# Optimization experiments

Measured on AMD Instinct MI355X. Metric: run time of the kernel, lower is better.

Reference implementation:

```python
import jax, jax.numpy as jnp
import numpy as np

B, S, DK, H = 4, 4096, 768, 64

def setup_inputs() -> dict:
    key = jax.random.key(0)
    ks = jax.random.split(key, 5)
    scale = 1.0 / np.sqrt(DK)
    x = jax.random.normal(ks[0], (B, S, DK), dtype=jnp.float32)
    Wq = jax.random.normal(ks[1], (H, DK), dtype=jnp.float32) * scale
    bq = jnp.zeros((H,), dtype=jnp.float32)
    Wv = jax.random.normal(ks[2], (H, DK), dtype=jnp.float32) * scale
    bv = jnp.zeros((H,), dtype=jnp.float32)
    return {"x": x, "Wq": Wq, "bq": bq, "Wv": Wv, "bv": bv}

def reference(x, Wq, bq, Wv, bv):
    # Faithful to source: k uses the QUERY projection (source bug), scale = d_k**-0.5 with d_k = input dim
    dk = x.shape[-1]
    q = jnp.einsum('bsd,hd->bsh', x, Wq) + bq  # [B,S,H]
    k = jnp.einsum('bsd,hd->bsh', x, Wq) + bq  # same projection as q
    v = jnp.einsum('bsd,hd->bsh', x, Wv) + bv
    score = jnp.einsum('bqh,bkh->bqk', q, k) * (dk ** -0.5)  # [B,S,S]
    prob = jax.nn.softmax(score, axis=-1)
    out = jnp.einsum('bqk,bkh->bqh', prob, v)  # [B,S,H]
    return out
```

## Files before the change

### kernel.cpp

```cpp
#include <hip/hip_runtime.h>
#include <hip/hip_bf16.h>
#include <stdint.h>
#include <math.h>


typedef unsigned short u16;
typedef __attribute__((ext_vector_type(8))) short bf16x8;
typedef __attribute__((ext_vector_type(4))) float f32x4;

#define MFMA16(a,b,c) __builtin_amdgcn_mfma_f32_16x16x32_bf16((a),(b),(c),0,0,0)

__device__ __forceinline__ u16 f2bf(float f) {
  union { float f; uint32_t u; } v; v.f = f;
  uint32_t u = v.u;
  return (u16)((u + 0x7FFFu + ((u >> 16) & 1u)) >> 16);
}

__device__ __forceinline__ bf16x8 ldsfrag(const u16* lds, int row, int k) {
  return *(const bf16x8*)(lds + row * 64 + (k ^ ((row & 7) << 3)));
}

__device__ __forceinline__ void gload_lds16(const void* g, void* l) {
  __builtin_amdgcn_global_load_lds(
      (__attribute__((address_space(1))) void*)g,
      (__attribute__((address_space(3))) void*)l, 16, 0, 0);
}

struct Regs { float4 r[12]; };

__device__ __forceinline__ void issue_loads(Regs& R, const float* xp,
                                            const float* qp, const float* vp,
                                            int ks) {
  const float4* a = (const float4*)(xp + (ks << 6));
  const float4* b = (const float4*)(qp + (ks << 6));
  const float4* c = (const float4*)(vp + (ks << 6));
  R.r[0] = a[0]; R.r[1] = a[1]; R.r[2] = a[2]; R.r[3] = a[3];
  R.r[4] = b[0]; R.r[5] = b[1]; R.r[6] = b[2]; R.r[7] = b[3];
  R.r[8] = c[0]; R.r[9] = c[1]; R.r[10] = c[2]; R.r[11] = c[3];
}

__device__ __forceinline__ void cvt8(const float4& a, const float4& b, bf16x8& o) {
  o[0] = (short)f2bf(a.x); o[1] = (short)f2bf(a.y);
  o[2] = (short)f2bf(a.z); o[3] = (short)f2bf(a.w);
  o[4] = (short)f2bf(b.x); o[5] = (short)f2bf(b.y);
  o[6] = (short)f2bf(b.z); o[7] = (short)f2bf(b.w);
}

__device__ __forceinline__ void cvt_store(const Regs& R, u16* xrow, u16* qrow,
                                          u16* vrow, int scol, int xsw) {
  bf16x8 lo, hi;
  cvt8(R.r[0], R.r[1], lo);  cvt8(R.r[2], R.r[3], hi);
  *(bf16x8*)(xrow + (scol ^ xsw)) = lo;
  *(bf16x8*)(xrow + ((scol + 8) ^ xsw)) = hi;
  cvt8(R.r[4], R.r[5], lo);  cvt8(R.r[6], R.r[7], hi);
  *(bf16x8*)(qrow + (scol ^ xsw)) = lo;
  *(bf16x8*)(qrow + ((scol + 8) ^ xsw)) = hi;
  cvt8(R.r[8], R.r[9], lo);  cvt8(R.r[10], R.r[11], hi);
  *(bf16x8*)(vrow + (scol ^ xsw)) = lo;
  *(bf16x8*)(vrow + ((scol + 8) ^ xsw)) = hi;
}

__global__ __launch_bounds__(256) void proj_k(
    const float* __restrict__ x, const float* __restrict__ Wq,
    const float* __restrict__ bq, const float* __restrict__ Wv,
    const float* __restrict__ bv, u16* __restrict__ qbf,
    u16* __restrict__ vtbf, float qscale)
{
  __shared__ __align__(16) u16 xs[2][4096];
  __shared__ __align__(16) u16 wqs[2][4096];
  __shared__ __align__(16) u16 wvs[2][4096];
  const int tid = threadIdx.x;
  const int lane = tid & 63;
  const int w = tid >> 6;
  const int l15 = lane & 15, lg = lane >> 4;
  const int s0 = blockIdx.x * 64;

  f32x4 acc[2][4];
#pragma unroll
  for (int i = 0; i < 2; i++)
#pragma unroll
    for (int n = 0; n < 4; n++) acc[i][n] = (f32x4){0.f, 0.f, 0.f, 0.f};

  const int srow = tid >> 2;
  const int scol = (tid & 3) << 4;
  const int xsw = (srow & 7) << 3;
  const float* xsrc = x + (size_t)(s0 + srow) * 768 + scol;
  const float* qsrc = Wq + (size_t)srow * 768 + scol;
  const float* vsrc = Wv + (size_t)srow * 768 + scol;

  Regs A, B;
  issue_loads(A, xsrc, qsrc, vsrc, 0);
  issue_loads(B, xsrc, qsrc, vsrc, 1);
  asm volatile("s_waitcnt vmcnt(12)" ::: "memory");
  cvt_store(A, &xs[0][srow * 64], &wqs[0][srow * 64], &wvs[0][srow * 64], scol, xsw);

#pragma unroll
  for (int ks = 0; ks < 12; ++ks) {
    const int b = ks & 1;
    if (ks + 2 < 12) {
      if (b) issue_loads(B, xsrc, qsrc, vsrc, ks + 2);
      else   issue_loads(A, xsrc, qsrc, vsrc, ks + 2);
    }
    asm volatile("s_waitcnt lgkmcnt(0)" ::: "memory");
    __builtin_amdgcn_s_barrier();
    __builtin_amdgcn_sched_barrier(0);

    const u16* xt = xs[b];
    const u16* qt = wqs[b];
    const u16* vt = wvs[b];
#pragma unroll
    for (int kk = 0; kk < 2; ++kk) {
      const int k = kk * 32 + lg * 8;
      if (w < 2) {
        bf16x8 a0 = ldsfrag(xt, (2 * w + 0) * 16 + l15, k);
        bf16x8 a1 = ldsfrag(xt, (2 * w + 1) * 16 + l15, k);
#pragma unroll
        for (int n = 0; n < 4; n++) {
          bf16x8 bb = ldsfrag(qt, n * 16 + l15, k);
          acc[0][n] = MFMA16(a0, bb, acc[0][n]);
          acc[1][n] = MFMA16(a1, bb, acc[1][n]);
        }
      } else {
        bf16x8 a0 = ldsfrag(vt, (2 * (w - 2) + 0) * 16 + l15, k);
        bf16x8 a1 = ldsfrag(vt, (2 * (w - 2) + 1) * 16 + l15, k);
#pragma unroll
        for (int n = 0; n < 4; n++) {
          bf16x8 bb = ldsfrag(xt, n * 16 + l15, k);
          acc[0][n] = MFMA16(a0, bb, acc[0][n]);
          acc[1][n] = MFMA16(a1, bb, acc[1][n]);
        }
      }
    }
    if (ks + 1 < 12) {
      if (ks < 10) asm volatile("s_waitcnt vmcnt(12)" ::: "memory");
      else         asm volatile("s_waitcnt vmcnt(0)" ::: "memory");
      u16* xd = &xs[b ^ 1][srow * 64];
      u16* qd = &wqs[b ^ 1][srow * 64];
      u16* vd = &wvs[b ^ 1][srow * 64];
      if (b) cvt_store(A, xd, qd, vd, scol, xsw);
      else   cvt_store(B, xd, qd, vd, scol, xsw);
    }
  }

  if (w < 2) {
#pragma unroll
    for (int i = 0; i < 2; i++)
#pragma unroll
      for (int n = 0; n < 4; n++) {
        const int h = n * 16 + l15;
        const float bias = bq[h];
#pragma unroll
        for (int r = 0; r < 4; r++) {
          const int sg = s0 + (2 * w + i) * 16 + lg * 4 + r;
          qbf[(size_t)sg * 64 + h] = f2bf((acc[i][n][r] + bias) * qscale);
        }
      }
  } else {
    const int b = s0 >> 12;
    const int sloc = s0 & 4095;
#pragma unroll
    for (int i = 0; i < 2; i++)
#pragma unroll
      for (int n = 0; n < 4; n++) {
        const int scg = sloc + n * 16 + l15;
#pragma unroll
        for (int r = 0; r < 4; r++) {
          const int h = (2 * (w - 2) + i) * 16 + lg * 4 + r;
          vtbf[(size_t)(b * 64 + h) * 4096 + scg] = f2bf(acc[i][n][r] + bv[h]);
        }
      }
  }
}

__global__ __launch_bounds__(512) void attn_k(
    const u16* __restrict__ qbf, const u16* __restrict__ vtbf,
    float* __restrict__ out)
{
  __shared__ __align__(16) u16 smem[3 * 8192 + 8 * 640];
  u16* pl = smem + 3 * 8192;
  const int tid = threadIdx.x;
  const int lane = tid & 63;
  const int w = tid >> 6;
  const int wq = w & 3, wk = w >> 2;
  const int l15 = lane & 15, lg = lane >> 4;
  const int b = blockIdx.y;
  const int q0 = blockIdx.x << 6;

  bf16x8 qf[2];
  {
    const u16* qr = qbf + (size_t)(b * 4096 + q0 + wq * 16 + l15) * 64 + lg * 8;
    qf[0] = *(const bf16x8*)(qr);
    qf[1] = *(const bf16x8*)(qr + 32);
  }

  f32x4 oacc[4];
#pragma unroll
  for (int i = 0; i < 4; i++) oacc[i] = (f32x4){0.f, 0.f, 0.f, 0.f};
  float lacc[4] = {0.f, 0.f, 0.f, 0.f};

  const int o = tid << 4;
  const int krow = o >> 7;
  const int ksw = o ^ ((krow & 7) << 4);
  const char* kbase = (const char*)qbf + (size_t)(b * 4096) * 128;
  const char* vbase = (const char*)vtbf + (size_t)(b * 64 + krow) * 8192 + (ksw & 127);

  const int NT = 64;
  auto stage = [&](int t, int s3) {
    char* kd = (char*)smem + s3 * 16384 + o;
    gload_lds16(kbase + (size_t)t * 8192 + ksw, kd);
    gload_lds16(vbase + t * 128, kd + 8192);
  };

  stage(0, 0);
  stage(1, 1);

  int sl = 0, sp = 2;
  for (int t = 0; t < NT; ++t) {
    if (t < NT - 1) asm volatile("s_waitcnt vmcnt(2)" ::: "memory");
    else            asm volatile("s_waitcnt vmcnt(0)" ::: "memory");
    __builtin_amdgcn_s_barrier();
    __builtin_amdgcn_sched_barrier(0);
    if (t + 2 < NT) stage(t + 2, sp);

    const u16* kt = smem + sl * 8192;
    const u16* vt = kt + 4096;

    f32x4 sc0 = (f32x4){0.f, 0.f, 0.f, 0.f}, sc1 = sc0;
    __builtin_amdgcn_s_setprio(1);
#pragma unroll
    for (int j = 0; j < 2; j++) {
      const int dk = j * 32 + lg * 8;
      bf16x8 k0f = ldsfrag(kt, wk * 32 + l15, dk);
      bf16x8 k1f = ldsfrag(kt, wk * 32 + 16 + l15, dk);
      sc0 = MFMA16(qf[j], k0f, sc0);
      sc1 = MFMA16(qf[j], k1f, sc1);
    }
    __builtin_amdgcn_s_setprio(0);
    float p0[4], p1[4], rs[4];
#pragma unroll
    for (int r = 0; r < 4; r++) {
      p0[r] = __expf(sc0[r]);
      p1[r] = __expf(sc1[r]);
      rs[r] = p0[r] + p1[r];
    }
#pragma unroll
    for (int m = 1; m < 16; m <<= 1)
#pragma unroll
      for (int r = 0; r < 4; r++) rs[r] += __shfl_xor(rs[r], m, 64);
#pragma unroll
    for (int r = 0; r < 4; r++) lacc[r] += rs[r];
    u16* pw = pl + w * 640;
#pragma unroll
    for (int r = 0; r < 4; r++) {
      pw[(lg * 4 + r) * 40 + l15]      = f2bf(p0[r]);
      pw[(lg * 4 + r) * 40 + 16 + l15] = f2bf(p1[r]);
    }
    asm volatile("s_waitcnt lgkmcnt(0)" ::: "memory");
    bf16x8 pf = *(const bf16x8*)(pw + l15 * 40 + lg * 8);
    __builtin_amdgcn_s_setprio(1);
#pragma unroll
    for (int db = 0; db < 4; ++db) {
      bf16x8 vf = ldsfrag(vt, db * 16 + l15, wk * 32 + lg * 8);
      oacc[db] = MFMA16(pf, vf, oacc[db]);
    }
    __builtin_amdgcn_s_setprio(0);

    sl = (sl == 2) ? 0 : sl + 1;
    sp = (sp == 2) ? 0 : sp + 1;
  }

  __syncthreads();
  float* oc = (float*)smem;
  float* lc = oc + 4 * 16 * 68;
  if (wk == 1) {
#pragma unroll
    for (int db = 0; db < 4; ++db)
#pragma unroll
      for (int r = 0; r < 4; r++)
        oc[(wq * 16 + lg * 4 + r) * 68 + db * 16 + l15] = oacc[db][r];
#pragma unroll
    for (int r = 0; r < 4; r++) lc[wq * 16 + lg * 4 + r] = lacc[r];
  }
  __syncthreads();
  if (wk == 0) {
#pragma unroll
    for (int db = 0; db < 4; ++db)
#pragma unroll
      for (int r = 0; r < 4; r++) {
        const int row = lg * 4 + r;
        const float ov = oacc[db][r] + oc[(wq * 16 + row) * 68 + db * 16 + l15];
        const float lt = lacc[r] + lc[wq * 16 + row];
        out[(size_t)(b * 4096 + q0 + wq * 16 + row) * 64 + db * 16 + l15] = ov / lt;
      }
  }
}

extern "C" void kernel_launch(void* const* d_in, const int* in_sizes, int n_in,
                              void* d_out, int out_size, void* d_ws, size_t ws_size,
                              hipStream_t stream) {
  const float* x  = (const float*)d_in[0];
  const float* Wq = (const float*)d_in[1];
  const float* bq = (const float*)d_in[2];
  const float* Wv = (const float*)d_in[3];
  const float* bv = (const float*)d_in[4];
  float* out = (float*)d_out;
  u16* qbf  = (u16*)d_ws;
  u16* vtbf = qbf + (size_t)16384 * 64;
  const float qscale = 1.0f / sqrtf(sqrtf(768.0f));
  proj_k<<<dim3(256), dim3(256), 0, stream>>>(x, Wq, bq, Wv, bv, qbf, vtbf, qscale);
  attn_k<<<dim3(64, 4), dim3(512), 0, stream>>>(qbf, vtbf, out);
}
```

Measured before the change: 165.6 us.

## Split attention over KV chunks with atomic accumulation and separate normalize kernel

The attention kernel now splits the 4096 keys into four chunks per query tile of 128 rows. Blocks use 256 threads, and the block-to-batch mapping is chosen to spread work across XCDs. Partial outputs and row sums go to global memory with atomicAdd, followed by a normalization kernel and two memsets. The projection kernel is also re-tiled to 32 rows per block to double the grid. This buys more parallelism and removes the cross-wave LDS reduction, at the cost of atomic traffic, extra launches and memsets, and nondeterministic summation order.

Result: faster. 153.0 us (-7.6%).

```diff
diff --git a/kernel.cpp b/kernel.cpp
--- a/kernel.cpp
+++ b/kernel.cpp
@@ -15,6 +15,9 @@
   uint32_t u = v.u;
   return (u16)((u + 0x7FFFu + ((u >> 16) & 1u)) >> 16);
 }
+__device__ __forceinline__ uint32_t pack2(float a, float b) {
+  return (uint32_t)f2bf(a) | ((uint32_t)f2bf(b) << 16);
+}
 
 __device__ __forceinline__ bf16x8 ldsfrag(const u16* lds, int row, int k) {
   return *(const bf16x8*)(lds + row * 64 + (k ^ ((row & 7) << 3)));
@@ -26,38 +29,22 @@
       (__attribute__((address_space(3))) void*)l, 16, 0, 0);
 }
 
-struct Regs { float4 r[12]; };
-
-__device__ __forceinline__ void issue_loads(Regs& R, const float* xp,
-                                            const float* qp, const float* vp,
-                                            int ks) {
-  const float4* a = (const float4*)(xp + (ks << 6));
-  const float4* b = (const float4*)(qp + (ks << 6));
-  const float4* c = (const float4*)(vp + (ks << 6));
-  R.r[0] = a[0]; R.r[1] = a[1]; R.r[2] = a[2]; R.r[3] = a[3];
-  R.r[4] = b[0]; R.r[5] = b[1]; R.r[6] = b[2]; R.r[7] = b[3];
-  R.r[8] = c[0]; R.r[9] = c[1]; R.r[10] = c[2]; R.r[11] = c[3];
-}
-
+struct PR { float4 xr[2]; float4 qr[4]; float4 vr[4]; };
+
+__device__ __forceinline__ void loadPR(PR& R, const float* xs_, const float* qs_,
+                                       const float* vs_, int ks) {
+  const float4* a = (const float4*)(xs_ + (ks << 6));
+  const float4* b = (const float4*)(qs_ + (ks << 6));
+  const float4* c = (const float4*)(vs_ + (ks << 6));
+  R.xr[0] = a[0]; R.xr[1] = a[1];
+  R.qr[0] = b[0]; R.qr[1] = b[1]; R.qr[2] = b[2]; R.qr[3] = b[3];
+  R.vr[0] = c[0]; R.vr[1] = c[1]; R.vr[2] = c[2]; R.vr[3] = c[3];
+}
 __device__ __forceinline__ void cvt8(const float4& a, const float4& b, bf16x8& o) {
   o[0] = (short)f2bf(a.x); o[1] = (short)f2bf(a.y);
   o[2] = (short)f2bf(a.z); o[3] = (short)f2bf(a.w);
   o[4] = (short)f2bf(b.x); o[5] = (short)f2bf(b.y);
   o[6] = (short)f2bf(b.z); o[7] = (short)f2bf(b.w);
-}
-
-__device__ __forceinline__ void cvt_store(const Regs& R, u16* xrow, u16* qrow,
-                                          u16* vrow, int scol, int xsw) {
-  bf16x8 lo, hi;
-  cvt8(R.r[0], R.r[1], lo);  cvt8(R.r[2], R.r[3], hi);
-  *(bf16x8*)(xrow + (scol ^ xsw)) = lo;
-  *(bf16x8*)(xrow + ((scol + 8) ^ xsw)) = hi;
-  cvt8(R.r[4], R.r[5], lo);  cvt8(R.r[6], R.r[7], hi);
-  *(bf16x8*)(qrow + (scol ^ xsw)) = lo;
-  *(bf16x8*)(qrow + ((scol + 8) ^ xsw)) = hi;
-  cvt8(R.r[8], R.r[9], lo);  cvt8(R.r[10], R.r[11], hi);
-  *(bf16x8*)(vrow + (scol ^ xsw)) = lo;
-  *(bf16x8*)(vrow + ((scol + 8) ^ xsw)) = hi;
 }
 
 __global__ __launch_bounds__(256) void proj_k(
@@ -66,232 +53,275 @@
     const float* __restrict__ bv, u16* __restrict__ qbf,
     u16* __restrict__ vtbf, float qscale)
 {
-  __shared__ __align__(16) u16 xs[2][4096];
-  __shared__ __align__(16) u16 wqs[2][4096];
-  __shared__ __align__(16) u16 wvs[2][4096];
+  __shared__ __align__(16) u16 xs[2][32 * 64];
+  __shared__ __align__(16) u16 wqs[2][64 * 64];
+  __shared__ __align__(16) u16 wvs[2][64 * 64];
   const int tid = threadIdx.x;
   const int lane = tid & 63;
   const int w = tid >> 6;
   const int l15 = lane & 15, lg = lane >> 4;
-  const int s0 = blockIdx.x * 64;
-
-  f32x4 acc[2][4];
-#pragma unroll
-  for (int i = 0; i < 2; i++)
-#pragma unroll
-    for (int n = 0; n < 4; n++) acc[i][n] = (f32x4){0.f, 0.f, 0.f, 0.f};
-
-  const int srow = tid >> 2;
-  const int scol = (tid & 3) << 4;
-  const int xsw = (srow & 7) << 3;
-  const float* xsrc = x + (size_t)(s0 + srow) * 768 + scol;
-  const float* qsrc = Wq + (size_t)srow * 768 + scol;
-  const float* vsrc = Wv + (size_t)srow * 768 + scol;
-
-  Regs A, B;
-  issue_loads(A, xsrc, qsrc, vsrc, 0);
-  issue_loads(B, xsrc, qsrc, vsrc, 1);
-  asm volatile("s_waitcnt vmcnt(12)" ::: "memory");
-  cvt_store(A, &xs[0][srow * 64], &wqs[0][srow * 64], &wvs[0][srow * 64], scol, xsw);
-
-#pragma unroll
-  for (int ks = 0; ks < 12; ++ks) {
-    const int b = ks & 1;
-    if (ks + 2 < 12) {
-      if (b) issue_loads(B, xsrc, qsrc, vsrc, ks + 2);
-      else   issue_loads(A, xsrc, qsrc, vsrc, ks + 2);
+  const int s0 = blockIdx.x * 32;
+
+  const int xrow = tid >> 3, xcol = (tid & 7) << 3;
+  const int wrow = tid >> 2, wcol = (tid & 3) << 4;
+  const int xswz = (xrow & 7) << 3;
+  const int wswz = (wrow & 7) << 3;
+  const float* xsrc = x + (size_t)(s0 + xrow) * 768 + xcol;
+  const float* qsrc = Wq + (size_t)wrow * 768 + wcol;
+  const float* vsrc = Wv + (size_t)wrow * 768 + wcol;
+
+  const f32x4 Z4 = {0.f, 0.f, 0.f, 0.f};
+  f32x4 acc[4];
+#pragma unroll
+  for (int n = 0; n < 4; n++) acc[n] = Z4;
+
+  PR A, B;
+  loadPR(A, xsrc, qsrc, vsrc, 0);
+
+  auto storePR = [&](const PR& R, int buf) {
+    bf16x8 t0, t1;
+    cvt8(R.xr[0], R.xr[1], t0);
+    *(bf16x8*)(&xs[buf][xrow * 64] + (xcol ^ xswz)) = t0;
+    cvt8(R.qr[0], R.qr[1], t0); cvt8(R.qr[2], R.qr[3], t1);
+    *(bf16x8*)(&wqs[buf][wrow * 64] + (wcol ^ wswz)) = t0;
+    *(bf16x8*)(&wqs[buf][wrow * 64] + ((wcol + 8) ^ wswz)) = t1;
+    cvt8(R.vr[0], R.vr[1], t0); cvt8(R.vr[2], R.vr[3], t1);
+    *(bf16x8*)(&wvs[buf][wrow * 64] + (wcol ^ wswz)) = t0;
+    *(bf16x8*)(&wvs[buf][wrow * 64] + ((wcol + 8) ^ wswz)) = t1;
+  };
+
+  auto mfma_phase = [&](int buf) {
+#pragma unroll
+    for (int kk = 0; kk < 2; ++kk) {
+      const int k = kk * 32 + lg * 8;
+      if (w < 2) {
+        bf16x8 a = ldsfrag(xs[buf], w * 16 + l15, k);
+#pragma unroll
+        for (int n = 0; n < 4; n++) {
+          bf16x8 bb = ldsfrag(wqs[buf], n * 16 + l15, k);
+          acc[n] = MFMA16(a, bb, acc[n]);
+        }
+      } else {
+        const int hb = (w - 2) * 32;
+        bf16x8 a0 = ldsfrag(wvs[buf], hb + l15, k);
+        bf16x8 a1 = ldsfrag(wvs[buf], hb + 16 + l15, k);
+        bf16x8 b0 = ldsfrag(xs[buf], l15, k);
+        bf16x8 b1 = ldsfrag(xs[buf], 16 + l15, k);
+        acc[0] = MFMA16(a0, b0, acc[0]);
+        acc[1] = MFMA16(a0, b1, acc[1]);
+        acc[2] = MFMA16(a1, b0, acc[2]);
+        acc[3] = MFMA16(a1, b1, acc[3]);
+      }
     }
+  };
+
+#pragma unroll
+  for (int kh = 0; kh < 6; ++kh) {
+    const int ks = kh * 2;
+    loadPR(B, xsrc, qsrc, vsrc, ks + 1);
+    storePR(A, 0);
     asm volatile("s_waitcnt lgkmcnt(0)" ::: "memory");
     __builtin_amdgcn_s_barrier();
     __builtin_amdgcn_sched_barrier(0);
-
-    const u16* xt = xs[b];
-    const u16* qt = wqs[b];
-    const u16* vt = wvs[b];
-#pragma unroll
-    for (int kk = 0; kk < 2; ++kk) {
-      const int k = kk * 32 + lg * 8;
-      if (w < 2) {
-        bf16x8 a0 = ldsfrag(xt, (2 * w + 0) * 16 + l15, k);
-        bf16x8 a1 = ldsfrag(xt, (2 * w + 1) * 16 + l15, k);
-#pragma unroll
-        for (int n = 0; n < 4; n++) {
-          bf16x8 bb = ldsfrag(qt, n * 16 + l15, k);
-          acc[0][n] = MFMA16(a0, bb, acc[0][n]);
-          acc[1][n] = MFMA16(a1, bb, acc[1][n]);
+    mfma_phase(0);
+    if (ks + 2 < 12) loadPR(A, xsrc, qsrc, vsrc, ks + 2);
+    storePR(B, 1);
+    asm volatile("s_waitcnt lgkmcnt(0)" ::: "memory");
+    __builtin_amdgcn_s_barrier();
+    __builtin_amdgcn_sched_barrier(0);
+    mfma_phase(1);
+  }
+
+  if (w < 2) {
+#pragma unroll
+    for (int n = 0; n < 4; n++) {
+      const int h = n * 16 + l15;
+      const float bias = bq[h];
+#pragma unroll
+      for (int r = 0; r < 4; r++) {
+        const int sg = s0 + w * 16 + lg * 4 + r;
+        qbf[(size_t)sg * 64 + h] = f2bf((acc[n][r] + bias) * qscale);
+      }
+    }
+  } else {
+    const int bb = s0 >> 12;
+    const int sloc = s0 & 4095;
+#pragma unroll
+    for (int mm = 0; mm < 2; mm++)
+#pragma unroll
+      for (int nn = 0; nn < 2; nn++) {
+        const int scg = sloc + nn * 16 + l15;
+#pragma unroll
+        for (int r = 0; r < 4; r++) {
+          const int h = (w - 2) * 32 + mm * 16 + lg * 4 + r;
+          vtbf[(size_t)(bb * 64 + h) * 4096 + scg] = f2bf(acc[mm * 2 + nn][r] + bv[h]);
         }
-      } else {
-        bf16x8 a0 = ldsfrag(vt, (2 * (w - 2) + 0) * 16 + l15, k);
-        bf16x8 a1 = ldsfrag(vt, (2 * (w - 2) + 1) * 16 + l15, k);
-#pragma unroll
-        for (int n = 0; n < 4; n++) {
-          bf16x8 bb = ldsfrag(xt, n * 16 + l15, k);
-          acc[0][n] = MFMA16(a0, bb, acc[0][n]);
-          acc[1][n] = MFMA16(a1, bb, acc[1][n]);
-        }
-      }
-    }
-    if (ks + 1 < 12) {
-      if (ks < 10) asm volatile("s_waitcnt vmcnt(12)" ::: "memory");
-      else         asm volatile("s_waitcnt vmcnt(0)" ::: "memory");
-      u16* xd = &xs[b ^ 1][srow * 64];
-      u16* qd = &wqs[b ^ 1][srow * 64];
-      u16* vd = &wvs[b ^ 1][srow * 64];
-      if (b) cvt_store(A, xd, qd, vd, scol, xsw);
-      else   cvt_store(B, xd, qd, vd, scol, xsw);
-    }
-  }
-
-  if (w < 2) {
-#pragma unroll
-    for (int i = 0; i < 2; i++)
-#pragma unroll
-      for (int n = 0; n < 4; n++) {
-        const int h = n * 16 + l15;
-        const float bias = bq[h];
-#pragma unroll
-        for (int r = 0; r < 4; r++) {
-          const int sg = s0 + (2 * w + i) * 16 + lg * 4 + r;
-          qbf[(size_t)sg * 64 + h] = f2bf((acc[i][n][r] + bias) * qscale);
-        }
-      }
-  } else {
-    const int b = s0 >> 12;
-    const int sloc = s0 & 4095;
-#pragma unroll
-    for (int i = 0; i < 2; i++)
-#pragma unroll
-      for (int n = 0; n < 4; n++) {
-        const int scg = sloc + n * 16 + l15;
-#pragma unroll
-        for (int r = 0; r < 4; r++) {
-          const int h = (2 * (w - 2) + i) * 16 + lg * 4 + r;
-          vtbf[(size_t)(b * 64 + h) * 4096 + scg] = f2bf(acc[i][n][r] + bv[h]);
-        }
-      }
-  }
-}
-
-__global__ __launch_bounds__(512) void attn_k(
+      }
+  }
+}
+
+__global__ __launch_bounds__(256) void attn_k(
     const u16* __restrict__ qbf, const u16* __restrict__ vtbf,
-    float* __restrict__ out)
+    float* __restrict__ o_acc, float* __restrict__ l_acc)
 {
-  __shared__ __align__(16) u16 smem[3 * 8192 + 8 * 640];
-  u16* pl = smem + 3 * 8192;
+  __shared__ __align__(16) u16 smem[3 * 4096 + 4 * 1280];
+  u16* pbuf = smem + 12288;
+  const int bid = blockIdx.x;
+  const int xcd = bid & 7;
+  const int batch = xcd >> 1;
+  const int j = bid >> 3;
+  const int qt = j >> 1;
+  const int sp = ((j & 1) << 1) | (xcd & 1);
+  const int q0 = qt << 7;
+  const int kvb = sp << 10;
+
   const int tid = threadIdx.x;
   const int lane = tid & 63;
   const int w = tid >> 6;
-  const int wq = w & 3, wk = w >> 2;
   const int l15 = lane & 15, lg = lane >> 4;
-  const int b = blockIdx.y;
-  const int q0 = blockIdx.x << 6;
-
-  bf16x8 qf[2];
-  {
-    const u16* qr = qbf + (size_t)(b * 4096 + q0 + wq * 16 + l15) * 64 + lg * 8;
-    qf[0] = *(const bf16x8*)(qr);
-    qf[1] = *(const bf16x8*)(qr + 32);
-  }
-
-  f32x4 oacc[4];
-#pragma unroll
-  for (int i = 0; i < 4; i++) oacc[i] = (f32x4){0.f, 0.f, 0.f, 0.f};
-  float lacc[4] = {0.f, 0.f, 0.f, 0.f};
+  const f32x4 Z4 = {0.f, 0.f, 0.f, 0.f};
+
+  bf16x8 qf[2][2];
+#pragma unroll
+  for (int nn = 0; nn < 2; nn++) {
+    const u16* qr = qbf + (size_t)(batch * 4096 + q0 + w * 32 + nn * 16 + l15) * 64 + lg * 8;
+    qf[nn][0] = *(const bf16x8*)(qr);
+    qf[nn][1] = *(const bf16x8*)(qr + 32);
+  }
+  asm volatile("s_waitcnt vmcnt(0)" ::: "memory");
+
+  f32x4 oacc[2][4];
+#pragma unroll
+  for (int nn = 0; nn < 2; nn++)
+#pragma unroll
+    for (int dd = 0; dd < 4; dd++) oacc[nn][dd] = Z4;
+  float lacc[2] = {0.f, 0.f};
 
   const int o = tid << 4;
   const int krow = o >> 7;
-  const int ksw = o ^ ((krow & 7) << 4);
-  const char* kbase = (const char*)qbf + (size_t)(b * 4096) * 128;
-  const char* vbase = (const char*)vtbf + (size_t)(b * 64 + krow) * 8192 + (ksw & 127);
-
-  const int NT = 64;
+  const int vrow = o >> 6;
+  const int koff = (o & 127) ^ ((krow & 7) << 4);
+  const int voff = (o & 63) ^ ((vrow & 3) << 4);
+  const char* ksrc = (const char*)qbf +
+      ((size_t)(batch * 4096 + kvb + krow)) * 128 + koff;
+  const char* vsrc = (const char*)vtbf +
+      ((size_t)(batch * 64 + vrow)) * 8192 + kvb * 2 + voff;
+
   auto stage = [&](int t, int s3) {
-    char* kd = (char*)smem + s3 * 16384 + o;
-    gload_lds16(kbase + (size_t)t * 8192 + ksw, kd);
-    gload_lds16(vbase + t * 128, kd + 8192);
+    char* d = (char*)smem + s3 * 8192 + o;
+    gload_lds16(ksrc + (size_t)t * 4096, d);
+    gload_lds16(vsrc + t * 64, d + 4096);
   };
 
   stage(0, 0);
   stage(1, 1);
 
-  int sl = 0, sp = 2;
-  for (int t = 0; t < NT; ++t) {
-    if (t < NT - 1) asm volatile("s_waitcnt vmcnt(2)" ::: "memory");
-    else            asm volatile("s_waitcnt vmcnt(0)" ::: "memory");
+  int sl = 0, sp3 = 2;
+  for (int t = 0; t < 32; ++t) {
+    if (t < 31) asm volatile("s_waitcnt vmcnt(2)" ::: "memory");
+    else        asm volatile("s_waitcnt vmcnt(0)" ::: "memory");
     __builtin_amdgcn_s_barrier();
     __builtin_amdgcn_sched_barrier(0);
-    if (t + 2 < NT) stage(t + 2, sp);
-
-    const u16* kt = smem + sl * 8192;
-    const u16* vt = kt + 4096;
-
-    f32x4 sc0 = (f32x4){0.f, 0.f, 0.f, 0.f}, sc1 = sc0;
+    if (t + 2 < 32) stage(t + 2, sp3);
+
+    const u16* kt = smem + sl * 4096;
+    const u16* vt = kt + 2048;
+
+    bf16x8 kf[2][2];
+#pragma unroll
+    for (int mm = 0; mm < 2; mm++)
+#pragma unroll
+      for (int kk = 0; kk < 2; kk++)
+        kf[mm][kk] = ldsfrag(kt, mm * 16 + l15, kk * 32 + lg * 8);
+    f32x4 sc[2][2];
     __builtin_amdgcn_s_setprio(1);
 #pragma unroll
-    for (int j = 0; j < 2; j++) {
-      const int dk = j * 32 + lg * 8;
-      bf16x8 k0f = ldsfrag(kt, wk * 32 + l15, dk);
-      bf16x8 k1f = ldsfrag(kt, wk * 32 + 16 + l15, dk);
-      sc0 = MFMA16(qf[j], k0f, sc0);
-      sc1 = MFMA16(qf[j], k1f, sc1);
+    for (int mm = 0; mm < 2; mm++)
+#pragma unroll
+      for (int nn = 0; nn < 2; nn++) {
+        f32x4 s = MFMA16(kf[mm][0], qf[nn][0], Z4);
+        sc[mm][nn] = MFMA16(kf[mm][1], qf[nn][1], s);
+      }
+    __builtin_amdgcn_s_setprio(0);
+
+    uint32_t pk[2][2][2];
+#pragma unroll
+    for (int nn = 0; nn < 2; nn++) {
+      float s = 0.f;
+#pragma unroll
+      for (int mm = 0; mm < 2; mm++) {
+        float e0 = __expf(sc[mm][nn][0]), e1 = __expf(sc[mm][nn][1]);
+        float e2 = __expf(sc[mm][nn][2]), e3 = __expf(sc[mm][nn][3]);
+        s += (e0 + e1) + (e2 + e3);
+        pk[nn][mm][0] = pack2(e0, e1);
+        pk[nn][mm][1] = pack2(e2, e3);
+      }
+      lacc[nn] += s;
     }
+
+    u16* pw = pbuf + w * 1280;
+#pragma unroll
+    for (int nn = 0; nn < 2; nn++)
+#pragma unroll
+      for (int mm = 0; mm < 2; mm++) {
+        uint2 v; v.x = pk[nn][mm][0]; v.y = pk[nn][mm][1];
+        *(uint2*)(pw + nn * 640 + l15 * 40 + mm * 16 + lg * 4) = v;
+      }
+    asm volatile("s_waitcnt lgkmcnt(0)" ::: "memory");
+    __builtin_amdgcn_sched_barrier(0);
+    bf16x8 pa[2];
+#pragma unroll
+    for (int nn = 0; nn < 2; nn++)
+      pa[nn] = *(const bf16x8*)(pw + nn * 640 + l15 * 40 + lg * 8);
+
+    bf16x8 vf[4];
+#pragma unroll
+    for (int dd = 0; dd < 4; dd++) {
+      const int row = dd * 16 + l15;
+      vf[dd] = *(const bf16x8*)(vt + row * 32 + ((lg * 8) ^ ((row & 3) << 3)));
+    }
+    __builtin_amdgcn_s_setprio(1);
+#pragma unroll
+    for (int nn = 0; nn < 2; nn++)
+#pragma unroll
+      for (int dd = 0; dd < 4; dd++)
+        oacc[nn][dd] = MFMA16(pa[nn], vf[dd], oacc[nn][dd]);
     __builtin_amdgcn_s_setprio(0);
-    float p0[4], p1[4], rs[4];
-#pragma unroll
-    for (int r = 0; r < 4; r++) {
-      p0[r] = __expf(sc0[r]);
-      p1[r] = __expf(sc1[r]);
-      rs[r] = p0[r] + p1[r];
-    }
-#pragma unroll
-    for (int m = 1; m < 16; m <<= 1)
-#pragma unroll
-      for (int r = 0; r < 4; r++) rs[r] += __shfl_xor(rs[r], m, 64);
-#pragma unroll
-    for (int r = 0; r < 4; r++) lacc[r] += rs[r];
-    u16* pw = pl + w * 640;
-#pragma unroll
-    for (int r = 0; r < 4; r++) {
-      pw[(lg * 4 + r) * 40 + l15]      = f2bf(p0[r]);
-      pw[(lg * 4 + r) * 40 + 16 + l15] = f2bf(p1[r]);
-    }
-    asm volatile("s_waitcnt lgkmcnt(0)" ::: "memory");
-    bf16x8 pf = *(const bf16x8*)(pw + l15 * 40 + lg * 8);
-    __builtin_amdgcn_s_setprio(1);
-#pragma unroll
-    for (int db = 0; db < 4; ++db) {
-      bf16x8 vf = ldsfrag(vt, db * 16 + l15, wk * 32 + lg * 8);
-      oacc[db] = MFMA16(pf, vf, oacc[db]);
-    }
-    __builtin_amdgcn_s_setprio(0);
 
     sl = (sl == 2) ? 0 : sl + 1;
-    sp = (sp == 2) ? 0 : sp + 1;
-  }
-
-  __syncthreads();
-  float* oc = (float*)smem;
-  float* lc = oc + 4 * 16 * 68;
-  if (wk == 1) {
-#pragma unroll
-    for (int db = 0; db < 4; ++db)
-#pragma unroll
-      for (int r = 0; r < 4; r++)
-        oc[(wq * 16 + lg * 4 + r) * 68 + db * 16 + l15] = oacc[db][r];
-#pragma unroll
-    for (int r = 0; r < 4; r++) lc[wq * 16 + lg * 4 + r] = lacc[r];
-  }
-  __syncthreads();
-  if (wk == 0) {
-#pragma unroll
-    for (int db = 0; db < 4; ++db)
+    sp3 = (sp3 == 2) ? 0 : sp3 + 1;
+  }
+
+#pragma unroll
+  for (int nn = 0; nn < 2; nn++) {
+    float s = lacc[nn];
+    s += __shfl_xor(s, 16);
+    s += __shfl_xor(s, 32);
+    if (lg == 0)
+      atomicAdd(&l_acc[batch * 4096 + q0 + w * 32 + nn * 16 + l15], s);
+  }
+#pragma unroll
+  for (int nn = 0; nn < 2; nn++)
+#pragma unroll
+    for (int dd = 0; dd < 4; dd++)
 #pragma unroll
       for (int r = 0; r < 4; r++) {
-        const int row = lg * 4 + r;
-        const float ov = oacc[db][r] + oc[(wq * 16 + row) * 68 + db * 16 + l15];
-        const float lt = lacc[r] + lc[wq * 16 + row];
-        out[(size_t)(b * 4096 + q0 + wq * 16 + row) * 64 + db * 16 + l15] = ov / lt;
-      }
+        const int qrow = q0 + w * 32 + nn * 16 + lg * 4 + r;
+        atomicAdd(&o_acc[(size_t)(batch * 4096 + qrow) * 64 + dd * 16 + l15],
+                  oacc[nn][dd][r]);
+      }
+}
+
+__global__ __launch_bounds__(256) void norm_k(float* __restrict__ out,
+                                              const float* __restrict__ l_acc) {
+  const size_t base = ((size_t)blockIdx.x * 256 + threadIdx.x) * 16;
+  const float inv = 1.0f / l_acc[base >> 6];
+  float4* p = (float4*)(out + base);
+#pragma unroll
+  for (int j = 0; j < 4; j++) {
+    float4 v = p[j];
+    v.x *= inv; v.y *= inv; v.z *= inv; v.w *= inv;
+    p[j] = v;
   }
 }
 
@@ -306,7 +336,12 @@
   float* out = (float*)d_out;
   u16* qbf  = (u16*)d_ws;
   u16* vtbf = qbf + (size_t)16384 * 64;
+  float* l_acc = (float*)((char*)d_ws + 4u * 1024 * 1024);
   const float qscale = 1.0f / sqrtf(sqrtf(768.0f));
-  proj_k<<<dim3(256), dim3(256), 0, stream>>>(x, Wq, bq, Wv, bv, qbf, vtbf, qscale);
-  attn_k<<<dim3(64, 4), dim3(512), 0, stream>>>(qbf, vtbf, out);
-}
+
+  (void)hipMemsetAsync(d_out, 0, (size_t)4 * 4096 * 64 * sizeof(float), stream);
+  (void)hipMemsetAsync(l_acc, 0, (size_t)16384 * sizeof(float), stream);
+  proj_k<<<dim3(512), dim3(256), 0, stream>>>(x, Wq, bq, Wv, bv, qbf, vtbf, qscale);
+  attn_k<<<dim3(512), dim3(256), 0, stream>>>(qbf, vtbf, out, l_acc);
+  norm_k<<<dim3(256), dim3(256), 0, stream>>>(out, l_acc);
+}
```
